# Performance work log

Hardware: AMD Instinct MI355X
Metric: run time of the kernel (lower is better)

Reference implementation:

```python
import jax, jax.numpy as jnp
import numpy as np

N = 100000      # nodes
E = 1600000     # edges (avg degree 16)
R = 8           # relations
D_IN = 128
D_HID = 128
D_OUT = 128


def setup_inputs() -> dict:
    key = jax.random.key(0)
    ks = jax.random.split(key, 10)
    s = 1.0 / np.sqrt(D_IN)
    return {
        "x": jax.random.normal(ks[0], (N, D_IN), dtype=jnp.float32),
        "edge_index": jax.random.randint(ks[1], (2, E), 0, N, dtype=jnp.int64),
        "edge_type": jax.random.randint(ks[2], (E,), 0, R, dtype=jnp.int64),
        "W1": jax.random.normal(ks[3], (R, D_IN, D_HID), dtype=jnp.float32) * s,
        "root1": jax.random.normal(ks[4], (D_IN, D_HID), dtype=jnp.float32) * s,
        "b1": jnp.zeros((D_HID,), dtype=jnp.float32),
        "W2": jax.random.normal(ks[5], (R, D_HID, D_OUT), dtype=jnp.float32) * s,
        "root2": jax.random.normal(ks[6], (D_HID, D_OUT), dtype=jnp.float32) * s,
        "b2": jnp.zeros((D_OUT,), dtype=jnp.float32),
    }


def _rgcn_conv(x, src, dst, et, W, root, b):
    """PyG-style RGCNConv: h_i = x_i @ root + b + sum_r mean_{j in N_r(i)} x_j @ W_r."""
    n = x.shape[0]
    r = W.shape[0]
    # transform all nodes once per relation: [R, N, out]
    xr = jnp.einsum('ni,rio->rno', x, W)
    msg = xr[et, src]                               # [E, out] gather per edge
    # per-(dst, relation) in-degree for mean aggregation
    key = dst * r + et
    cnt = jax.ops.segment_sum(jnp.ones((et.shape[0],), jnp.float32), key,
                              num_segments=n * r)
    norm = 1.0 / jnp.maximum(cnt[key], 1.0)         # [E]
    agg = jax.ops.segment_sum(msg * norm[:, None], dst, num_segments=n)
    return agg + x @ root + b


def reference(x, edge_index, edge_type, W1, root1, b1, W2, root2, b2):
    src, dst = edge_index[0], edge_index[1]
    h = _rgcn_conv(x, src, dst, edge_type, W1, root1, b1)
    h = jax.nn.relu(h)   # dropout is identity in eval mode
    h = _rgcn_conv(h, src, dst, edge_type, W2, root2, b2)
    return h
```

## Files before the change

### kernel.cpp

```cpp
#include <hip/hip_runtime.h>

#define NN 100000
#define NE 1600000
#define NR 8
#define DD 128
#define NKEY (NN * NR)
#define NBLK ((NKEY + 1023) / 1024)
#define RSTRIDE 580

typedef __attribute__((ext_vector_type(8))) short short8;
typedef __attribute__((ext_vector_type(4))) float f32x4;

__device__ __forceinline__ float bf2f(unsigned short u) {
  union { unsigned int i; float f; } c; c.i = ((unsigned int)u) << 16; return c.f;
}
__device__ __forceinline__ unsigned short f2bf(float f) {
  union { float f; unsigned int i; } c; c.f = f;
  unsigned int u = c.i;
  return (unsigned short)((u + 0x7FFFu + ((u >> 16) & 1u)) >> 16);
}

__global__ __launch_bounds__(256) void k_prep(
    const float* __restrict__ x, unsigned short* __restrict__ xb,
    const float* __restrict__ W1, const float* __restrict__ root1,
    const float* __restrict__ W2, const float* __restrict__ root2,
    unsigned short* __restrict__ wbf, int* __restrict__ cnt) {
  const int CAST_B = (NN * DD / 4 + 255) / 256;
  const int ZERO_B = (NKEY + 255) / 256;
  int b = blockIdx.x, t = threadIdx.x;
  if (b < CAST_B) {
    int i = b * 256 + t;
    if (i < NN * DD / 4) {
      float4 f = ((const float4*)x)[i];
      ushort4 u;
      u.x = f2bf(f.x); u.y = f2bf(f.y); u.z = f2bf(f.z); u.w = f2bf(f.w);
      ((ushort4*)xb)[i] = u;
    }
  } else if (b < CAST_B + ZERO_B) {
    int i = (b - CAST_B) * 256 + t;
    if (i < NKEY) cnt[i] = 0;
  } else {
    int idx = (b - CAST_B - ZERO_B) * 256 + t;
    int layer = idx / (9 * 16384);
    int rem = idx % (9 * 16384);
    int r = rem / 16384;
    int nk = rem % 16384;
    int n = nk >> 7, k = nk & 127;
    float v;
    if (r < 8) v = (layer ? W2 : W1)[r * 16384 + k * 128 + n];
    else       v = (layer ? root2 : root1)[k * 128 + n];
    wbf[idx] = f2bf(v);
  }
}

__global__ __launch_bounds__(256) void k_count(
    const int* __restrict__ ei, const int* __restrict__ et,
    int* __restrict__ cnt, int* __restrict__ rank) {
  int e = blockIdx.x * 256 + threadIdx.x;
  if (e < NE) {
    int dst = ei[NE + e];
    int r = et[e];
    rank[e] = atomicAdd(&cnt[dst * NR + r], 1);
  }
}

__global__ __launch_bounds__(1024) void k_scan1(
    const int* __restrict__ cnt, int* __restrict__ offs, int* __restrict__ bsum) {
  __shared__ int sw[16];
  int t = threadIdx.x, b = blockIdx.x;
  int lane = t & 63, wid = t >> 6;
  int i = b * 1024 + t;
  int v = (i < NKEY) ? cnt[i] : 0;
  int x = v;
#pragma unroll
  for (int o = 1; o < 64; o <<= 1) {
    int y = __shfl_up(x, o);
    if (lane >= o) x += y;
  }
  if (lane == 63) sw[wid] = x;
  __syncthreads();
  if (wid == 0) {
    int s = (lane < 16) ? sw[lane] : 0;
#pragma unroll
    for (int o = 1; o < 16; o <<= 1) {
      int y = __shfl_up(s, o);
      if (lane >= o) s += y;
    }
    if (lane < 16) sw[lane] = s;
  }
  __syncthreads();
  int base = (wid > 0) ? sw[wid - 1] : 0;
  if (i < NKEY) offs[i] = base + x - v;
  if (t == 1023) bsum[b] = base + x;
}

__global__ __launch_bounds__(1024) void k_scan2(int* __restrict__ bsum) {
  __shared__ int sw[16];
  int t = threadIdx.x;
  int lane = t & 63, wid = t >> 6;
  int v = (t < NBLK) ? bsum[t] : 0;
  int x = v;
#pragma unroll
  for (int o = 1; o < 64; o <<= 1) {
    int y = __shfl_up(x, o);
    if (lane >= o) x += y;
  }
  if (lane == 63) sw[wid] = x;
  __syncthreads();
  if (wid == 0) {
    int s = (lane < 16) ? sw[lane] : 0;
#pragma unroll
    for (int o = 1; o < 16; o <<= 1) {
      int y = __shfl_up(s, o);
      if (lane >= o) s += y;
    }
    if (lane < 16) sw[lane] = s;
  }
  __syncthreads();
  int base = (wid > 0) ? sw[wid - 1] : 0;
  if (t < NBLK) bsum[t] = base + x - v;
}

__global__ __launch_bounds__(256) void k_scan3(
    int* __restrict__ offs, const int* __restrict__ bsum, int* __restrict__ csr) {
  int i = blockIdx.x * 256 + threadIdx.x;
  if (i < NKEY) offs[i] += bsum[i >> 10];
  if (i == 0) offs[NKEY] = NE;
  if (i < 192) csr[NE + i] = 0;
}

__global__ __launch_bounds__(256) void k_csr(
    const int* __restrict__ ei, const int* __restrict__ et,
    const int* __restrict__ offs, const int* __restrict__ rank,
    int* __restrict__ csr) {
  int e = blockIdx.x * 256 + threadIdx.x;
  if (e < NE) {
    int src = ei[e];
    int key = ei[NE + e] * NR + et[e];
    csr[offs[key] + rank[e]] = src;
  }
}

template <int RELU, int OUTBF>
__global__ __launch_bounds__(512, 4) void k_fused(
    const unsigned short* __restrict__ xb,
    const unsigned short* __restrict__ wl,
    const int* __restrict__ offs, const int* __restrict__ csr,
    const float* __restrict__ bias, void* __restrict__ outp) {
  __shared__ unsigned int sAgg32[32 * RSTRIDE];
  const unsigned short* sAggH = (const unsigned short*)sAgg32;

  const int tid = threadIdx.x;
  const int w = tid >> 6;
  const int lane = tid & 63;
  const int m = lane & 15, q = lane >> 4;
  const int n0 = blockIdx.x * 32;
  const int k0 = n0 * NR;

  int oidx = k0 + 32 * w + lane;
  if (oidx > NKEY) oidx = NKEY;
  const int offv = offs[oidx];
  const int p0 = __builtin_amdgcn_readlane(offv, 0);
  const int p1 = __builtin_amdgcn_readlane(offv, 32);

#pragma unroll
  for (int i = 0; i < 4; i++) {
    int node = 4 * w + i;
    unsigned int v = *(const unsigned int*)(xb + (size_t)(n0 + node) * DD + 2 * lane);
    sAgg32[node * RSTRIDE + 8 * 64 + lane] = v;
  }

  int kloc = 0;
  int kbeg = p0;
  int kend = __builtin_amdgcn_readlane(offv, 1);
  float ax = 0.f, ay = 0.f;

  int wbase = p0;
  int pv0 = csr[wbase + lane];
  int pv1 = csr[wbase + 64 + lane];

#define ISSUE8(DST, NB) do {                                                 \
    if ((NB) - wbase == 64) {                                                \
      wbase += 64; pv0 = pv1; pv1 = csr[wbase + 64 + lane];                  \
    }                                                                        \
    const int ib_ = (NB) - wbase;                                            \
    _Pragma("unroll") for (int j_ = 0; j_ < 8; j_++) {                       \
      unsigned s_ = (unsigned)__builtin_amdgcn_readlane(pv0, ib_ + j_);      \
      (DST)[j_] = *(const ushort2*)(xb + (size_t)s_ * DD + 2 * lane);        \
    }                                                                        \
  } while (0)

#define CONSUME8(V, B0) do {                                                 \
    _Pragma("unroll") for (int j_ = 0; j_ < 8; j_++) {                       \
      if ((B0) + j_ < p1) {                                                  \
        while ((B0) + j_ >= kend) {                                          \
          float nm_ = __builtin_amdgcn_rcpf(fmaxf((float)(kend - kbeg), 1.f)); \
          unsigned lo_ = f2bf(ax * nm_), hi_ = f2bf(ay * nm_);               \
          int node_ = 4 * w + (kloc >> 3);                                   \
          sAgg32[node_ * RSTRIDE + (kloc & 7) * 64 + lane] = lo_ | (hi_ << 16); \
          ax = 0.f; ay = 0.f;                                                \
          kloc++;                                                            \
          kbeg = kend;                                                       \
          kend = __builtin_amdgcn_readlane(offv, kloc + 1);                  \
        }                                                                    \
        ax += bf2f((V)[j_].x);                                               \
        ay += bf2f((V)[j_].y);                                               \
      }                                                                      \
    }                                                                        \
  } while (0)

  ushort2 va[8], vb[8];
  ISSUE8(va, p0);

  for (int base = p0; base < p1; base += 16) {
    ISSUE8(vb, base + 8);
    CONSUME8(va, base);
    ISSUE8(va, base + 16);
    CONSUME8(vb, base + 8);
  }
  while (kloc < 32) {
    float nm = __builtin_amdgcn_rcpf(fmaxf((float)(kend - kbeg), 1.f));
    unsigned lo = f2bf(ax * nm), hi = f2bf(ay * nm);
    int node = 4 * w + (kloc >> 3);
    sAgg32[node * RSTRIDE + (kloc & 7) * 64 + lane] = lo | (hi << 16);
    ax = 0.f; ay = 0.f;
    kloc++;
    kbeg = kend;
    kend = (kloc < 32) ? __builtin_amdgcn_readlane(offv, kloc + 1) : kend;
  }
#undef ISSUE8
#undef CONSUME8
  __syncthreads();

  f32x4 acc0 = {0.f, 0.f, 0.f, 0.f};
  f32x4 acc1 = {0.f, 0.f, 0.f, 0.f};
  for (int mat = 0; mat < 9; mat++) {
    short8 a0[4], a1[4];
#pragma unroll
    for (int ks = 0; ks < 4; ks++) {
      a0[ks] = *(const short8*)(sAggH + m * (2 * RSTRIDE) + mat * 128 + ks * 32 + q * 8);
      a1[ks] = *(const short8*)(sAggH + (m + 16) * (2 * RSTRIDE) + mat * 128 + ks * 32 + q * 8);
    }
    const unsigned short* wr = wl + mat * DD * DD;
#pragma unroll
    for (int ks = 0; ks < 4; ks++) {
      short8 b = *(const short8*)(wr + (w * 16 + m) * DD + ks * 32 + q * 8);
      acc0 = __builtin_amdgcn_mfma_f32_16x16x32_bf16(a0[ks], b, acc0, 0, 0, 0);
      acc1 = __builtin_amdgcn_mfma_f32_16x16x32_bf16(a1[ks], b, acc1, 0, 0, 0);
    }
  }

  {
    const int c0 = w * 16 + m;
    const float bv = bias[c0];
#pragma unroll
    for (int i = 0; i < 4; i++) {
      int row0 = n0 + q * 4 + i;
      int row1 = row0 + 16;
      float v0 = acc0[i] + bv, v1 = acc1[i] + bv;
      if (RELU) { v0 = fmaxf(v0, 0.f); v1 = fmaxf(v1, 0.f); }
      if (OUTBF) {
        ((unsigned short*)outp)[(size_t)row0 * DD + c0] = f2bf(v0);
        ((unsigned short*)outp)[(size_t)row1 * DD + c0] = f2bf(v1);
      } else {
        ((float*)outp)[(size_t)row0 * DD + c0] = v0;
        ((float*)outp)[(size_t)row1 * DD + c0] = v1;
      }
    }
  }
}


extern "C" void kernel_launch(void* const* d_in, const int* in_sizes, int n_in,
                              void* d_out, int out_size, void* d_ws, size_t ws_size,
                              hipStream_t stream) {
  const float* x     = (const float*)d_in[0];
  const int*   ei    = (const int*)d_in[1];
  const int*   et    = (const int*)d_in[2];
  const float* W1    = (const float*)d_in[3];
  const float* root1 = (const float*)d_in[4];
  const float* b1    = (const float*)d_in[5];
  const float* W2    = (const float*)d_in[6];
  const float* root2 = (const float*)d_in[7];
  const float* b2    = (const float*)d_in[8];
  float* out = (float*)d_out;

  char* p = (char*)d_ws;
  unsigned short* xb1 = (unsigned short*)p; p += (size_t)NN * DD * 2;
  unsigned short* xb2 = (unsigned short*)p; p += (size_t)NN * DD * 2;
  unsigned short* wbf = (unsigned short*)p; p += (size_t)2 * 9 * DD * DD * 2;
  int* cnt  = (int*)p; p += (size_t)NKEY * 4;
  int* offs = (int*)p; p += (size_t)(NKEY + 16) * 4;
  int* bsum = (int*)p; p += (size_t)800 * 4;
  int* rank = (int*)p; p += (size_t)NE * 4;
  int* csr  = (int*)p; p += (size_t)(NE + 192) * 4;

  const int PREP_B = (NN * DD / 4 + 255) / 256 + (NKEY + 255) / 256 + (2 * 9 * 16384) / 256;
  k_prep<<<PREP_B, 256, 0, stream>>>(x, xb1, W1, root1, W2, root2, wbf, cnt);
  k_count<<<(NE + 255) / 256, 256, 0, stream>>>(ei, et, cnt, rank);
  k_scan1<<<NBLK, 1024, 0, stream>>>(cnt, offs, bsum);
  k_scan2<<<1, 1024, 0, stream>>>(bsum);
  k_scan3<<<(NKEY + 255) / 256, 256, 0, stream>>>(offs, bsum, csr);
  k_csr<<<(NE + 255) / 256, 256, 0, stream>>>(ei, et, offs, rank, csr);

  dim3 fgrid(NN / 32);
  k_fused<1, 1><<<fgrid, 512, 0, stream>>>(xb1, wbf, offs, csr, b1, (void*)xb2);
  k_fused<0, 0><<<fgrid, 512, 0, stream>>>(xb2, wbf + 9 * DD * DD, offs, csr, b2, (void*)out);
}
```

Before: 556.8 us.

## Pad CSR segments to multiples of four and gather 16-byte rows per quarter-wave

Each (dst,relation) segment in the CSR is padded to a multiple of 4 entries. Padding entries point to an extra zero row appended to the bf16 feature buffers. In the gather, each quarter-wave now loads a whole 16-byte slice (8 bf16) of a different neighbor, so one instruction fetches four edges instead of one 4-byte slice per lane. Partial sums are reduced across quarter-waves with shuffles at segment boundaries. The change cuts the number of gather instructions and uses wider loads, in exchange for padding traffic, extra CSR init work and shuffle reductions.

```diff
diff --git a/kernel.cpp b/kernel.cpp
--- a/kernel.cpp
+++ b/kernel.cpp
@@ -7,6 +7,7 @@
 #define NKEY (NN * NR)
 #define NBLK ((NKEY + 1023) / 1024)
 #define RSTRIDE 580
+#define CSRN 4000256
 
 typedef __attribute__((ext_vector_type(8))) short short8;
 typedef __attribute__((ext_vector_type(4))) float f32x4;
@@ -22,11 +23,15 @@
 
 __global__ __launch_bounds__(256) void k_prep(
     const float* __restrict__ x, unsigned short* __restrict__ xb,
+    unsigned short* __restrict__ xb2,
     const float* __restrict__ W1, const float* __restrict__ root1,
     const float* __restrict__ W2, const float* __restrict__ root2,
-    unsigned short* __restrict__ wbf, int* __restrict__ cnt) {
+    unsigned short* __restrict__ wbf, int* __restrict__ cnt,
+    int* __restrict__ csr) {
   const int CAST_B = (NN * DD / 4 + 255) / 256;
-  const int ZERO_B = (NKEY + 255) / 256;
+  const int ZROW_B = 1;
+  const int ZCNT_B = (NKEY + 255) / 256;
+  const int WT_B   = (2 * 9 * 16384) / 256;
   int b = blockIdx.x, t = threadIdx.x;
   if (b < CAST_B) {
     int i = b * 256 + t;
@@ -36,11 +41,14 @@
       u.x = f2bf(f.x); u.y = f2bf(f.y); u.z = f2bf(f.z); u.w = f2bf(f.w);
       ((ushort4*)xb)[i] = u;
     }
-  } else if (b < CAST_B + ZERO_B) {
-    int i = (b - CAST_B) * 256 + t;
+  } else if (b < CAST_B + ZROW_B) {
+    if (t < 64)       ((unsigned int*)(xb  + (size_t)NN * DD))[t]      = 0;
+    else if (t < 128) ((unsigned int*)(xb2 + (size_t)NN * DD))[t - 64] = 0;
+  } else if (b < CAST_B + ZROW_B + ZCNT_B) {
+    int i = (b - CAST_B - ZROW_B) * 256 + t;
     if (i < NKEY) cnt[i] = 0;
-  } else {
-    int idx = (b - CAST_B - ZERO_B) * 256 + t;
+  } else if (b < CAST_B + ZROW_B + ZCNT_B + WT_B) {
+    int idx = (b - CAST_B - ZROW_B - ZCNT_B) * 256 + t;
     int layer = idx / (9 * 16384);
     int rem = idx % (9 * 16384);
     int r = rem / 16384;
@@ -50,6 +58,9 @@
     if (r < 8) v = (layer ? W2 : W1)[r * 16384 + k * 128 + n];
     else       v = (layer ? root2 : root1)[k * 128 + n];
     wbf[idx] = f2bf(v);
+  } else {
+    int i = (b - CAST_B - ZROW_B - ZCNT_B - WT_B) * 256 + t;
+    if (i < CSRN) csr[i] = NN;
   }
 }
 
@@ -70,7 +81,7 @@
   int t = threadIdx.x, b = blockIdx.x;
   int lane = t & 63, wid = t >> 6;
   int i = b * 1024 + t;
-  int v = (i < NKEY) ? cnt[i] : 0;
+  int v = (i < NKEY) ? ((cnt[i] + 3) & ~3) : 0;
   int x = v;
 #pragma unroll
   for (int o = 1; o < 64; o <<= 1) {
@@ -122,11 +133,12 @@
 }
 
 __global__ __launch_bounds__(256) void k_scan3(
-    int* __restrict__ offs, const int* __restrict__ bsum, int* __restrict__ csr) {
+    int* __restrict__ offs, const int* __restrict__ bsum, const int* __restrict__ cnt) {
   int i = blockIdx.x * 256 + threadIdx.x;
-  if (i < NKEY) offs[i] += bsum[i >> 10];
-  if (i == 0) offs[NKEY] = NE;
-  if (i < 192) csr[NE + i] = 0;
+  if (i < NKEY) {
+    offs[i] += bsum[i >> 10];
+    if (i == NKEY - 1) offs[NKEY] = offs[i] + ((cnt[i] + 3) & ~3);
+  }
 }
 
 __global__ __launch_bounds__(256) void k_csr(
@@ -146,6 +158,7 @@
     const unsigned short* __restrict__ xb,
     const unsigned short* __restrict__ wl,
     const int* __restrict__ offs, const int* __restrict__ csr,
+    const int* __restrict__ cnt,
     const float* __restrict__ bias, void* __restrict__ outp) {
   __shared__ unsigned int sAgg32[32 * RSTRIDE];
   const unsigned short* sAggH = (const unsigned short*)sAgg32;
@@ -154,6 +167,8 @@
   const int w = tid >> 6;
   const int lane = tid & 63;
   const int m = lane & 15, q = lane >> 4;
+  const int qq = q;
+  const int dlo = (lane & 15) * 8;
   const int n0 = blockIdx.x * 32;
   const int k0 = n0 * NR;
 
@@ -162,6 +177,7 @@
   const int offv = offs[oidx];
   const int p0 = __builtin_amdgcn_readlane(offv, 0);
   const int p1 = __builtin_amdgcn_readlane(offv, 32);
+  const int tcv = cnt[k0 + 32 * w + (lane & 31)];
 
 #pragma unroll
   for (int i = 0; i < 4; i++) {
@@ -171,65 +187,68 @@
   }
 
   int kloc = 0;
-  int kbeg = p0;
   int kend = __builtin_amdgcn_readlane(offv, 1);
-  float ax = 0.f, ay = 0.f;
+  float acc[8] = {0.f, 0.f, 0.f, 0.f, 0.f, 0.f, 0.f, 0.f};
 
   int wbase = p0;
   int pv0 = csr[wbase + lane];
   int pv1 = csr[wbase + 64 + lane];
 
-#define ISSUE8(DST, NB) do {                                                 \
-    if ((NB) - wbase == 64) {                                                \
+#define ISSUE4(DST, POS) do {                                                \
+    if ((POS) - wbase == 64) {                                               \
       wbase += 64; pv0 = pv1; pv1 = csr[wbase + 64 + lane];                  \
     }                                                                        \
-    const int ib_ = (NB) - wbase;                                            \
-    _Pragma("unroll") for (int j_ = 0; j_ < 8; j_++) {                       \
-      unsigned s_ = (unsigned)__builtin_amdgcn_readlane(pv0, ib_ + j_);      \
-      (DST)[j_] = *(const ushort2*)(xb + (size_t)s_ * DD + 2 * lane);        \
+    int src_ = __shfl(pv0, (POS) - wbase + qq);                              \
+    (DST) = *(const short8*)(xb + (size_t)src_ * DD + dlo);                  \
+  } while (0)
+
+#define FLUSHK() do {                                                        \
+    _Pragma("unroll") for (int e_ = 0; e_ < 8; e_++) {                       \
+      acc[e_] += __shfl_xor(acc[e_], 16);                                    \
+      acc[e_] += __shfl_xor(acc[e_], 32);                                    \
+    }                                                                        \
+    float nm_ = __builtin_amdgcn_rcpf(                                       \
+        fmaxf((float)__builtin_amdgcn_readlane(tcv, kloc), 1.f));            \
+    if (qq == 0) {                                                           \
+      uint4 u_;                                                              \
+      u_.x = (unsigned)f2bf(acc[0]*nm_) | ((unsigned)f2bf(acc[1]*nm_) << 16);\
+      u_.y = (unsigned)f2bf(acc[2]*nm_) | ((unsigned)f2bf(acc[3]*nm_) << 16);\
+      u_.z = (unsigned)f2bf(acc[4]*nm_) | ((unsigned)f2bf(acc[5]*nm_) << 16);\
+      u_.w = (unsigned)f2bf(acc[6]*nm_) | ((unsigned)f2bf(acc[7]*nm_) << 16);\
+      int node_ = 4 * w + (kloc >> 3);                                       \
+      *(uint4*)&sAgg32[node_ * RSTRIDE + (kloc & 7) * 64 + 4 * m] = u_;      \
+    }                                                                        \
+    _Pragma("unroll") for (int e_ = 0; e_ < 8; e_++) acc[e_] = 0.f;          \
+    kloc++;                                                                  \
+    kend = __builtin_amdgcn_readlane(offv, kloc + 1);                        \
+  } while (0)
+
+#define CONSUME4(V, POS) do {                                                \
+    if ((POS) < p1) {                                                        \
+      while ((POS) >= kend) FLUSHK();                                        \
+      _Pragma("unroll") for (int e_ = 0; e_ < 8; e_++)                       \
+        acc[e_] += bf2f((unsigned short)(V)[e_]);                            \
     }                                                                        \
   } while (0)
 
-#define CONSUME8(V, B0) do {                                                 \
-    _Pragma("unroll") for (int j_ = 0; j_ < 8; j_++) {                       \
-      if ((B0) + j_ < p1) {                                                  \
-        while ((B0) + j_ >= kend) {                                          \
-          float nm_ = __builtin_amdgcn_rcpf(fmaxf((float)(kend - kbeg), 1.f)); \
-          unsigned lo_ = f2bf(ax * nm_), hi_ = f2bf(ay * nm_);               \
-          int node_ = 4 * w + (kloc >> 3);                                   \
-          sAgg32[node_ * RSTRIDE + (kloc & 7) * 64 + lane] = lo_ | (hi_ << 16); \
-          ax = 0.f; ay = 0.f;                                                \
-          kloc++;                                                            \
-          kbeg = kend;                                                       \
-          kend = __builtin_amdgcn_readlane(offv, kloc + 1);                  \
-        }                                                                    \
-        ax += bf2f((V)[j_].x);                                               \
-        ay += bf2f((V)[j_].y);                                               \
-      }                                                                      \
-    }                                                                        \
-  } while (0)
-
-  ushort2 va[8], vb[8];
-  ISSUE8(va, p0);
-
-  for (int base = p0; base < p1; base += 16) {
-    ISSUE8(vb, base + 8);
-    CONSUME8(va, base);
-    ISSUE8(va, base + 16);
-    CONSUME8(vb, base + 8);
-  }
-  while (kloc < 32) {
-    float nm = __builtin_amdgcn_rcpf(fmaxf((float)(kend - kbeg), 1.f));
-    unsigned lo = f2bf(ax * nm), hi = f2bf(ay * nm);
-    int node = 4 * w + (kloc >> 3);
-    sAgg32[node * RSTRIDE + (kloc & 7) * 64 + lane] = lo | (hi << 16);
-    ax = 0.f; ay = 0.f;
-    kloc++;
-    kbeg = kend;
-    kend = (kloc < 32) ? __builtin_amdgcn_readlane(offv, kloc + 1) : kend;
-  }
-#undef ISSUE8
-#undef CONSUME8
+  short8 va[4], vb[4];
+#pragma unroll
+  for (int j = 0; j < 4; j++) ISSUE4(va[j], p0 + 4 * j);
+
+  for (int base = p0; base < p1; base += 32) {
+#pragma unroll
+    for (int j = 0; j < 4; j++) ISSUE4(vb[j], base + 16 + 4 * j);
+#pragma unroll
+    for (int j = 0; j < 4; j++) CONSUME4(va[j], base + 4 * j);
+#pragma unroll
+    for (int j = 0; j < 4; j++) ISSUE4(va[j], base + 32 + 4 * j);
+#pragma unroll
+    for (int j = 0; j < 4; j++) CONSUME4(vb[j], base + 16 + 4 * j);
+  }
+  while (kloc < 32) FLUSHK();
+#undef ISSUE4
+#undef FLUSHK
+#undef CONSUME4
   __syncthreads();
 
   f32x4 acc0 = {0.f, 0.f, 0.f, 0.f};
@@ -286,24 +305,25 @@
   float* out = (float*)d_out;
 
   char* p = (char*)d_ws;
-  unsigned short* xb1 = (unsigned short*)p; p += (size_t)NN * DD * 2;
-  unsigned short* xb2 = (unsigned short*)p; p += (size_t)NN * DD * 2;
+  unsigned short* xb1 = (unsigned short*)p; p += (size_t)(NN + 1) * DD * 2;
+  unsigned short* xb2 = (unsigned short*)p; p += (size_t)(NN + 1) * DD * 2;
   unsigned short* wbf = (unsigned short*)p; p += (size_t)2 * 9 * DD * DD * 2;
   int* cnt  = (int*)p; p += (size_t)NKEY * 4;
   int* offs = (int*)p; p += (size_t)(NKEY + 16) * 4;
   int* bsum = (int*)p; p += (size_t)800 * 4;
   int* rank = (int*)p; p += (size_t)NE * 4;
-  int* csr  = (int*)p; p += (size_t)(NE + 192) * 4;
-
-  const int PREP_B = (NN * DD / 4 + 255) / 256 + (NKEY + 255) / 256 + (2 * 9 * 16384) / 256;
-  k_prep<<<PREP_B, 256, 0, stream>>>(x, xb1, W1, root1, W2, root2, wbf, cnt);
+  int* csr  = (int*)p; p += (size_t)CSRN * 4;
+
+  const int PREP_B = (NN * DD / 4 + 255) / 256 + 1 + (NKEY + 255) / 256 +
+                     (2 * 9 * 16384) / 256 + (CSRN + 255) / 256;
+  k_prep<<<PREP_B, 256, 0, stream>>>(x, xb1, xb2, W1, root1, W2, root2, wbf, cnt, csr);
   k_count<<<(NE + 255) / 256, 256, 0, stream>>>(ei, et, cnt, rank);
   k_scan1<<<NBLK, 1024, 0, stream>>>(cnt, offs, bsum);
   k_scan2<<<1, 1024, 0, stream>>>(bsum);
-  k_scan3<<<(NKEY + 255) / 256, 256, 0, stream>>>(offs, bsum, csr);
+  k_scan3<<<(NKEY + 255) / 256, 256, 0, stream>>>(offs, bsum, cnt);
   k_csr<<<(NE + 255) / 256, 256, 0, stream>>>(ei, et, offs, rank, csr);
 
   dim3 fgrid(NN / 32);
-  k_fused<1, 1><<<fgrid, 512, 0, stream>>>(xb1, wbf, offs, csr, b1, (void*)xb2);
-  k_fused<0, 0><<<fgrid, 512, 0, stream>>>(xb2, wbf + 9 * DD * DD, offs, csr, b2, (void*)out);
-}
+  k_fused<1, 1><<<fgrid, 512, 0, stream>>>(xb1, wbf, offs, csr, cnt, b1, (void*)xb2);
+  k_fused<0, 0><<<fgrid, 512, 0, stream>>>(xb2, wbf + 9 * DD * DD, offs, csr, cnt, b2, (void*)out);
+}
```

Result: slower. 704.4 us (+26.5%).

## Gather int8-quantized neighbor features in layer one and fuse count into prep

Applied to the files above, without the earlier changes.

Layer one's neighbor gather now reads per-node int8-quantized features plus a per-node scale, which is stored next to each CSR entry. This halves the gather bytes compared with bf16. The edge-count atomics are folded into the prep kernel, and the count zeroing moves to a memset. This adds an extra scale array written in the CSR build and lowers the precision of the layer-one aggregation, which risks accuracy.

```diff
diff --git a/kernel.cpp b/kernel.cpp
--- a/kernel.cpp
+++ b/kernel.cpp
@@ -19,28 +19,51 @@
   unsigned int u = c.i;
   return (unsigned short)((u + 0x7FFFu + ((u >> 16) & 1u)) >> 16);
 }
+__device__ __forceinline__ int qz(float v, float rs) {
+  int q = (int)rintf(v * rs);
+  return q > 127 ? 127 : (q < -127 ? -127 : q);
+}
+
+template <bool Q8> struct GTsel { using T = ushort2; };
+template <> struct GTsel<true> { using T = unsigned short; };
 
 __global__ __launch_bounds__(256) void k_prep(
     const float* __restrict__ x, unsigned short* __restrict__ xb,
+    unsigned char* __restrict__ x8, float* __restrict__ sc,
     const float* __restrict__ W1, const float* __restrict__ root1,
     const float* __restrict__ W2, const float* __restrict__ root2,
-    unsigned short* __restrict__ wbf, int* __restrict__ cnt) {
-  const int CAST_B = (NN * DD / 4 + 255) / 256;
-  const int ZERO_B = (NKEY + 255) / 256;
+    unsigned short* __restrict__ wbf, int* __restrict__ cnt,
+    const int* __restrict__ ei, const int* __restrict__ et,
+    int* __restrict__ rank) {
+  const int COUNT_B = (NE + 255) / 256;
+  const int CAST_B  = NN * DD / 4 / 256;
   int b = blockIdx.x, t = threadIdx.x;
-  if (b < CAST_B) {
-    int i = b * 256 + t;
-    if (i < NN * DD / 4) {
-      float4 f = ((const float4*)x)[i];
-      ushort4 u;
-      u.x = f2bf(f.x); u.y = f2bf(f.y); u.z = f2bf(f.z); u.w = f2bf(f.w);
-      ((ushort4*)xb)[i] = u;
-    }
-  } else if (b < CAST_B + ZERO_B) {
-    int i = (b - CAST_B) * 256 + t;
-    if (i < NKEY) cnt[i] = 0;
+  if (b < COUNT_B) {
+    int e = b * 256 + t;
+    if (e < NE) {
+      int dst = ei[NE + e];
+      int r = et[e];
+      rank[e] = atomicAdd(&cnt[dst * NR + r], 1);
+    }
+  } else if (b < COUNT_B + CAST_B) {
+    int i = (b - COUNT_B) * 256 + t;
+    float4 f = ((const float4*)x)[i];
+    ushort4 u;
+    u.x = f2bf(f.x); u.y = f2bf(f.y); u.z = f2bf(f.z); u.w = f2bf(f.w);
+    ((ushort4*)xb)[i] = u;
+    float m = fmaxf(fmaxf(fabsf(f.x), fabsf(f.y)), fmaxf(fabsf(f.z), fabsf(f.w)));
+#pragma unroll
+    for (int k = 1; k < 32; k <<= 1) m = fmaxf(m, __shfl_xor(m, k));
+    m = fmaxf(m, 1e-20f);
+    float s = m * (1.0f / 127.0f);
+    float rs = 127.0f / m;
+    int q0 = qz(f.x, rs), q1 = qz(f.y, rs), q2 = qz(f.z, rs), q3 = qz(f.w, rs);
+    unsigned int pk = (unsigned)(q0 & 0xff) | ((unsigned)(q1 & 0xff) << 8) |
+                      ((unsigned)(q2 & 0xff) << 16) | ((unsigned)(q3 & 0xff) << 24);
+    ((unsigned int*)x8)[i] = pk;
+    if ((t & 31) == 0) sc[i >> 5] = s;
   } else {
-    int idx = (b - CAST_B - ZERO_B) * 256 + t;
+    int idx = (b - COUNT_B - CAST_B) * 256 + t;
     int layer = idx / (9 * 16384);
     int rem = idx % (9 * 16384);
     int r = rem / 16384;
@@ -53,17 +76,6 @@
   }
 }
 
-__global__ __launch_bounds__(256) void k_count(
-    const int* __restrict__ ei, const int* __restrict__ et,
-    int* __restrict__ cnt, int* __restrict__ rank) {
-  int e = blockIdx.x * 256 + threadIdx.x;
-  if (e < NE) {
-    int dst = ei[NE + e];
-    int r = et[e];
-    rank[e] = atomicAdd(&cnt[dst * NR + r], 1);
-  }
-}
-
 __global__ __launch_bounds__(1024) void k_scan1(
     const int* __restrict__ cnt, int* __restrict__ offs, int* __restrict__ bsum) {
   __shared__ int sw[16];
@@ -122,28 +134,34 @@
 }
 
 __global__ __launch_bounds__(256) void k_scan3(
-    int* __restrict__ offs, const int* __restrict__ bsum, int* __restrict__ csr) {
+    int* __restrict__ offs, const int* __restrict__ bsum,
+    int* __restrict__ csr, float* __restrict__ csrs) {
   int i = blockIdx.x * 256 + threadIdx.x;
   if (i < NKEY) offs[i] += bsum[i >> 10];
   if (i == 0) offs[NKEY] = NE;
-  if (i < 192) csr[NE + i] = 0;
+  if (i < 192) { csr[NE + i] = 0; csrs[NE + i] = 0.f; }
 }
 
 __global__ __launch_bounds__(256) void k_csr(
     const int* __restrict__ ei, const int* __restrict__ et,
     const int* __restrict__ offs, const int* __restrict__ rank,
-    int* __restrict__ csr) {
+    const float* __restrict__ sc,
+    int* __restrict__ csr, float* __restrict__ csrs) {
   int e = blockIdx.x * 256 + threadIdx.x;
   if (e < NE) {
     int src = ei[e];
     int key = ei[NE + e] * NR + et[e];
-    csr[offs[key] + rank[e]] = src;
-  }
-}
-
-template <int RELU, int OUTBF>
+    int slot = offs[key] + rank[e];
+    csr[slot] = src;
+    csrs[slot] = sc[src];
+  }
+}
+
+template <int RELU, int OUTBF, int GQ8>
 __global__ __launch_bounds__(512, 4) void k_fused(
-    const unsigned short* __restrict__ xb,
+    const unsigned char* __restrict__ gx,
+    const float* __restrict__ gs,
+    const unsigned short* __restrict__ xbr,
     const unsigned short* __restrict__ wl,
     const int* __restrict__ offs, const int* __restrict__ csr,
     const float* __restrict__ bias, void* __restrict__ outp) {
@@ -166,7 +184,7 @@
 #pragma unroll
   for (int i = 0; i < 4; i++) {
     int node = 4 * w + i;
-    unsigned int v = *(const unsigned int*)(xb + (size_t)(n0 + node) * DD + 2 * lane);
+    unsigned int v = *(const unsigned int*)(xbr + (size_t)(n0 + node) * DD + 2 * lane);
     sAgg32[node * RSTRIDE + 8 * 64 + lane] = v;
   }
 
@@ -178,19 +196,31 @@
   int wbase = p0;
   int pv0 = csr[wbase + lane];
   int pv1 = csr[wbase + 64 + lane];
-
-#define ISSUE8(DST, NB) do {                                                 \
+  float sv0 = 0.f, sv1 = 0.f;
+  if constexpr (GQ8) {
+    sv0 = gs[wbase + lane];
+    sv1 = gs[wbase + 64 + lane];
+  }
+
+#define ISSUE8(DST, SD, NB) do {                                             \
     if ((NB) - wbase == 64) {                                                \
       wbase += 64; pv0 = pv1; pv1 = csr[wbase + 64 + lane];                  \
+      if constexpr (GQ8) { sv0 = sv1; sv1 = gs[wbase + 64 + lane]; }         \
     }                                                                        \
     const int ib_ = (NB) - wbase;                                            \
     _Pragma("unroll") for (int j_ = 0; j_ < 8; j_++) {                       \
       unsigned s_ = (unsigned)__builtin_amdgcn_readlane(pv0, ib_ + j_);      \
-      (DST)[j_] = *(const ushort2*)(xb + (size_t)s_ * DD + 2 * lane);        \
+      if constexpr (GQ8) {                                                   \
+        (DST)[j_] = *(const unsigned short*)(gx + (size_t)s_ * 128 + 2 * lane); \
+        (SD)[j_] = __uint_as_float(__builtin_amdgcn_readlane(                \
+            __float_as_uint(sv0), ib_ + j_));                                \
+      } else {                                                               \
+        (DST)[j_] = *(const ushort2*)(gx + (size_t)s_ * 256 + 4 * lane);     \
+      }                                                                      \
     }                                                                        \
   } while (0)
 
-#define CONSUME8(V, B0) do {                                                 \
+#define CONSUME8(V, S, B0) do {                                              \
     _Pragma("unroll") for (int j_ = 0; j_ < 8; j_++) {                       \
       if ((B0) + j_ < p1) {                                                  \
         while ((B0) + j_ >= kend) {                                          \
@@ -203,20 +233,27 @@
           kbeg = kend;                                                       \
           kend = __builtin_amdgcn_readlane(offv, kloc + 1);                  \
         }                                                                    \
-        ax += bf2f((V)[j_].x);                                               \
-        ay += bf2f((V)[j_].y);                                               \
+        if constexpr (GQ8) {                                                 \
+          unsigned u_ = (V)[j_];                                             \
+          ax += (S)[j_] * (float)(signed char)(u_ & 0xff);                   \
+          ay += (S)[j_] * (float)(signed char)(u_ >> 8);                     \
+        } else {                                                             \
+          ax += bf2f((V)[j_].x);                                             \
+          ay += bf2f((V)[j_].y);                                             \
+        }                                                                    \
       }                                                                      \
     }                                                                        \
   } while (0)
 
-  ushort2 va[8], vb[8];
-  ISSUE8(va, p0);
+  typename GTsel<GQ8 != 0>::T va[8], vb[8];
+  float sa[8], sb[8];
+  ISSUE8(va, sa, p0);
 
   for (int base = p0; base < p1; base += 16) {
-    ISSUE8(vb, base + 8);
-    CONSUME8(va, base);
-    ISSUE8(va, base + 16);
-    CONSUME8(vb, base + 8);
+    ISSUE8(vb, sb, base + 8);
+    CONSUME8(va, sa, base);
+    ISSUE8(va, sa, base + 16);
+    CONSUME8(vb, sb, base + 8);
   }
   while (kloc < 32) {
     float nm = __builtin_amdgcn_rcpf(fmaxf((float)(kend - kbeg), 1.f));
@@ -288,22 +325,30 @@
   char* p = (char*)d_ws;
   unsigned short* xb1 = (unsigned short*)p; p += (size_t)NN * DD * 2;
   unsigned short* xb2 = (unsigned short*)p; p += (size_t)NN * DD * 2;
+  unsigned char*  x8  = (unsigned char*)p;  p += (size_t)NN * DD;
+  float* sc = (float*)p; p += (size_t)NN * 4;
   unsigned short* wbf = (unsigned short*)p; p += (size_t)2 * 9 * DD * DD * 2;
   int* cnt  = (int*)p; p += (size_t)NKEY * 4;
   int* offs = (int*)p; p += (size_t)(NKEY + 16) * 4;
   int* bsum = (int*)p; p += (size_t)800 * 4;
   int* rank = (int*)p; p += (size_t)NE * 4;
   int* csr  = (int*)p; p += (size_t)(NE + 192) * 4;
-
-  const int PREP_B = (NN * DD / 4 + 255) / 256 + (NKEY + 255) / 256 + (2 * 9 * 16384) / 256;
-  k_prep<<<PREP_B, 256, 0, stream>>>(x, xb1, W1, root1, W2, root2, wbf, cnt);
-  k_count<<<(NE + 255) / 256, 256, 0, stream>>>(ei, et, cnt, rank);
+  float* csrs = (float*)p; p += (size_t)(NE + 192) * 4;
+
+  hipMemsetAsync(cnt, 0, (size_t)NKEY * 4, stream);
+
+  const int PREP_B = (NE + 255) / 256 + NN * DD / 4 / 256 + (2 * 9 * 16384) / 256;
+  k_prep<<<PREP_B, 256, 0, stream>>>(x, xb1, x8, sc, W1, root1, W2, root2, wbf,
+                                     cnt, ei, et, rank);
   k_scan1<<<NBLK, 1024, 0, stream>>>(cnt, offs, bsum);
   k_scan2<<<1, 1024, 0, stream>>>(bsum);
-  k_scan3<<<(NKEY + 255) / 256, 256, 0, stream>>>(offs, bsum, csr);
-  k_csr<<<(NE + 255) / 256, 256, 0, stream>>>(ei, et, offs, rank, csr);
+  k_scan3<<<(NKEY + 255) / 256, 256, 0, stream>>>(offs, bsum, csr, csrs);
+  k_csr<<<(NE + 255) / 256, 256, 0, stream>>>(ei, et, offs, rank, sc, csr, csrs);
 
   dim3 fgrid(NN / 32);
-  k_fused<1, 1><<<fgrid, 512, 0, stream>>>(xb1, wbf, offs, csr, b1, (void*)xb2);
-  k_fused<0, 0><<<fgrid, 512, 0, stream>>>(xb2, wbf + 9 * DD * DD, offs, csr, b2, (void*)out);
-}
+  k_fused<1, 1, 1><<<fgrid, 512, 0, stream>>>(x8, csrs, xb1, wbf, offs, csr,
+                                              b1, (void*)xb2);
+  k_fused<0, 0, 0><<<fgrid, 512, 0, stream>>>((const unsigned char*)xb2, csrs, xb2,
+                                              wbf + 9 * DD * DD, offs, csr,
+                                              b2, (void*)out);
+}
```

After: 593.7 us. +6.6%, slower.
